# Performance work log

Hardware: AMD Instinct MI355X
Metric: run time of the kernel (lower is better)

The kernel has to match this reference:

```python
import jax, jax.numpy as jnp
import numpy as np

N, E, F, H, O, R = 50000, 600000, 128, 128, 64, 8


def setup_inputs() -> dict:
    key = jax.random.key(0)
    ks = jax.random.split(key, 10)
    x = jax.random.normal(ks[0], (N, F), dtype=jnp.float32)
    edge_index = jax.random.randint(ks[1], (2, E), 0, N, dtype=jnp.int64)
    edge_weight = jax.random.uniform(ks[2], (E,), dtype=jnp.float32)
    edge_type = jax.random.randint(ks[3], (E,), 0, R, dtype=jnp.int64)
    s = 1.0 / np.sqrt(F)
    W1 = jax.random.uniform(ks[4], (R, F, H), jnp.float32, -s, s)
    root1 = jax.random.uniform(ks[5], (F, H), jnp.float32, -s, s)
    bias1 = jnp.zeros((H,), jnp.float32)
    sh = 1.0 / np.sqrt(H)
    W2 = jax.random.uniform(ks[6], (R, H, O), jnp.float32, -sh, sh)
    root2 = jax.random.uniform(ks[7], (H, O), jnp.float32, -sh, sh)
    bias2 = jnp.zeros((O,), jnp.float32)
    return {"x": x, "edge_index": edge_index, "edge_weight": edge_weight,
            "edge_type": edge_type, "W1": W1, "root1": root1, "bias1": bias1,
            "W2": W2, "root2": root2, "bias2": bias2}


def _rgcn_conv(x, src, dst, et, ew, W, root, bias, num_nodes):
    # project every node by every relation: [N, R, out] (cheaper than per-edge
    # materialization of weight[edge_type] which is E x in x out)
    proj = jnp.einsum('nd,rdo->nro', x, W)
    # per-edge message = x_j @ W[edge_type] * edge_weight  -> [E, out]
    msg = proj[src, et] * ew[:, None]
    # weighted scatter-mean over destination nodes
    agg = jax.ops.segment_sum(msg, dst, num_segments=num_nodes)
    cnt = jax.ops.segment_sum(jnp.ones_like(ew), dst, num_segments=num_nodes)
    agg = agg / jnp.maximum(cnt, 1.0)[:, None]
    # root (self) transform + bias
    return agg + x @ root + bias


def reference(x, edge_index, edge_weight, edge_type, W1, root1, bias1, W2, root2, bias2):
    src, dst = edge_index[0], edge_index[1]
    et = edge_type.astype(jnp.int32)
    # min-max normalize edge weights as in RGCN.forward
    ew = (edge_weight - edge_weight.min()) / (edge_weight.max() - edge_weight.min() + 1e-8)
    n = x.shape[0]
    h = jax.nn.relu(_rgcn_conv(x, src, dst, et, ew, W1, root1, bias1, n))
    return _rgcn_conv(h, src, dst, et, ew, W2, root2, bias2, n)
```

## Files before the change

kernel.cpp:

```cpp
#include <hip/hip_runtime.h>
#include <hip/hip_bf16.h>

#define F_DIM 128
#define H_DIM 128
#define O_DIM 64
#define R_NUM 8

typedef __attribute__((ext_vector_type(8))) short bf16x8;
typedef __attribute__((ext_vector_type(4))) float f32x4;
typedef __attribute__((ext_vector_type(8))) unsigned short u16x8;

union V8 { bf16x8 v; short4 h[2]; };

__device__ __forceinline__ unsigned short f2b(float f) {
    unsigned u = __float_as_uint(f);
    u += 0x7FFFu + ((u >> 16) & 1u);
    return (unsigned short)(u >> 16);
}
__device__ __forceinline__ unsigned f2b2(float lo, float hi) {
    union { __hip_bfloat162 h; unsigned u; } p;
    p.h = __float22bfloat162_rn(make_float2(lo, hi));
    return p.u;
}
__device__ __forceinline__ unsigned short f2b1(float f) {
    union { __hip_bfloat16 h; unsigned short u; } p;
    p.h = __float2bfloat16(f);
    return p.u;
}
__device__ __forceinline__ float b2f(unsigned short b) {
    return __uint_as_float(((unsigned)b) << 16);
}

__global__ __launch_bounds__(256) void setupA(
    const float* __restrict__ ew, const int* __restrict__ dst,
    const int* __restrict__ et, int E, int* __restrict__ deg2,
    float* __restrict__ bmn, float* __restrict__ bmx,
    const float* __restrict__ x, unsigned short* __restrict__ xb, long x4,
    const float* __restrict__ W1, const float* __restrict__ root1,
    const float* __restrict__ W2, const float* __restrict__ root2,
    unsigned short* __restrict__ wt1, unsigned short* __restrict__ wt2) {
    __shared__ float smn[256], smx[256];
    const int tid = threadIdx.x;
    const int gstride = gridDim.x * blockDim.x;
    int g0 = blockIdx.x * blockDim.x + tid;

    float mn = 1e30f, mx = -1e30f;
    for (int i = g0; i < E; i += gstride) {
        atomicAdd(&deg2[dst[i] * R_NUM + et[i]], 1);
        float v = ew[i];
        mn = fminf(mn, v);
        mx = fmaxf(mx, v);
    }
    smn[tid] = mn; smx[tid] = mx;
    __syncthreads();
    for (int s = 128; s > 0; s >>= 1) {
        if (tid < s) {
            smn[tid] = fminf(smn[tid], smn[tid + s]);
            smx[tid] = fmaxf(smx[tid], smx[tid + s]);
        }
        __syncthreads();
    }
    if (tid == 0) { bmn[blockIdx.x] = smn[0]; bmx[blockIdx.x] = smx[0]; }

    for (long i = g0; i < x4; i += gstride) {
        float4 v = ((const float4*)x)[i];
        uint2 o = make_uint2(f2b2(v.x, v.y), f2b2(v.z, v.w));
        ((uint2*)xb)[i] = o;
    }

    const int n1 = 9 * 128 * 128, n2 = 9 * 64 * 128;
    for (int idx = g0; idx < n1 + n2; idx += gstride) {
        if (idx < n1) {
            int r = idx / (128 * 128), rem = idx % (128 * 128);
            int n = rem / 128, k = rem % 128;
            float v = (r < 8) ? W1[((size_t)r * 128 + k) * 128 + n]
                              : root1[(size_t)k * 128 + n];
            wt1[idx] = f2b1(v);
        } else {
            int j = idx - n1;
            int r = j / (64 * 128), rem = j % (64 * 128);
            int n = rem / 128, k = rem % 128;
            float v = (r < 8) ? W2[((size_t)r * 128 + k) * 64 + n]
                              : root2[(size_t)k * 64 + n];
            wt2[j] = f2b1(v);
        }
    }
}

__global__ void scan1_kernel(const int* __restrict__ deg, int* __restrict__ rp,
                             int* __restrict__ bsum, float* __restrict__ invc,
                             int M, int N) {
    __shared__ int s[256];
    int base = blockIdx.x * 2048;
    int t = threadIdx.x;
    int v[8]; int loc = 0;
#pragma unroll
    for (int i = 0; i < 8; ++i) {
        int idx = base + t * 8 + i;
        v[i] = (idx < M) ? deg[idx] : 0;
        loc += v[i];
    }
    int node = blockIdx.x * 256 + t;
    if (node < N) invc[node] = 1.0f / (float)max(loc, 1);
    s[t] = loc;
    __syncthreads();
    for (int off = 1; off < 256; off <<= 1) {
        int x = (t >= off) ? s[t - off] : 0;
        __syncthreads();
        s[t] += x;
        __syncthreads();
    }
    int run = s[t] - loc;
#pragma unroll
    for (int i = 0; i < 8; ++i) {
        int idx = base + t * 8 + i;
        if (idx < M) rp[idx] = run;
        run += v[i];
    }
    if (t == 255) bsum[blockIdx.x] = s[255];
}

__global__ void scan2_mm(int* bsum, int nb, const float* __restrict__ bmn,
                         const float* __restrict__ bmx, float* mm) {
    __shared__ int s[256];
    __shared__ float smn[256], smx[256];
    int t = threadIdx.x;
    int v = (t < nb) ? bsum[t] : 0;
    s[t] = v;
    smn[t] = fminf(bmn[t], bmn[t + 256]);
    smx[t] = fmaxf(bmx[t], bmx[t + 256]);
    __syncthreads();
    for (int off = 1; off < 256; off <<= 1) {
        int x = (t >= off) ? s[t - off] : 0;
        __syncthreads();
        s[t] += x;
        __syncthreads();
    }
    if (t < nb) bsum[t] = s[t] - v;
    for (int r = 128; r > 0; r >>= 1) {
        if (t < r) {
            smn[t] = fminf(smn[t], smn[t + r]);
            smx[t] = fmaxf(smx[t], smx[t + r]);
        }
        __syncthreads();
    }
    if (t == 0) { mm[0] = smn[0]; mm[1] = smx[0]; }
}

__global__ void fill2_kernel(const int* __restrict__ src, const int* __restrict__ dst,
                             const int* __restrict__ et, const float* __restrict__ ew,
                             const float* __restrict__ mm, const float* __restrict__ invc,
                             int* __restrict__ rp2, const int* __restrict__ bsum,
                             unsigned* __restrict__ erec, int E) {
    int e = blockIdx.x * blockDim.x + threadIdx.x;
    if (e >= E) return;
    int d = dst[e];
    int i = d * R_NUM + et[e];
    int pos = atomicAdd(&rp2[i], 1) + bsum[i >> 11];
    float mn = mm[0], mx = mm[1];
    unsigned wq = f2b((ew[e] - mn) / (mx - mn + 1e-8f) * invc[d]);
    erec[pos] = (wq << 17) | (unsigned)src[e];
}

__global__ __launch_bounds__(256) void gather_y(
    const int* __restrict__ rp2, const int* __restrict__ bsum,
    const unsigned* __restrict__ erec,
    const unsigned short* __restrict__ inp,
    unsigned short* __restrict__ y, int N) {
    int gid = blockIdx.x * 256 + threadIdx.x;
    int seg = gid >> 4;
    int n = seg >> 3;
    if (n >= N) return;
    int j = (gid & 15) * 8;
    int beg = (seg == 0) ? 0 : rp2[seg - 1] + bsum[(seg - 1) >> 11];
    int end = rp2[seg] + bsum[seg >> 11];
    float acc[8] = {0.f, 0.f, 0.f, 0.f, 0.f, 0.f, 0.f, 0.f};
    int k = beg;
    for (; k + 2 <= end; k += 2) {
        unsigned r0 = erec[k], r1 = erec[k + 1];
        float w0 = __uint_as_float((r0 >> 1) & 0x7FFF8000u);
        float w1 = __uint_as_float((r1 >> 1) & 0x7FFF8000u);
        u16x8 v0 = *(const u16x8*)(inp + (size_t)(r0 & 0x1FFFFu) * 128 + j);
        u16x8 v1 = *(const u16x8*)(inp + (size_t)(r1 & 0x1FFFFu) * 128 + j);
#pragma unroll
        for (int c = 0; c < 8; ++c) acc[c] += w0 * b2f(v0[c]);
#pragma unroll
        for (int c = 0; c < 8; ++c) acc[c] += w1 * b2f(v1[c]);
    }
    if (k < end) {
        unsigned r0 = erec[k];
        float w0 = __uint_as_float((r0 >> 1) & 0x7FFF8000u);
        u16x8 v0 = *(const u16x8*)(inp + (size_t)(r0 & 0x1FFFFu) * 128 + j);
#pragma unroll
        for (int c = 0; c < 8; ++c) acc[c] += w0 * b2f(v0[c]);
    }
    uint4 ov = make_uint4(f2b2(acc[0], acc[1]), f2b2(acc[2], acc[3]),
                          f2b2(acc[4], acc[5]), f2b2(acc[6], acc[7]));
    *(uint4*)(y + ((size_t)(seg & 7) * N + (size_t)n) * 128 + j) = ov;
}

__global__ __launch_bounds__(512, 4) void gemm_y2(
    const unsigned short* __restrict__ y,
    const unsigned short* __restrict__ inp,
    const unsigned short* __restrict__ Wt,
    const float* __restrict__ bias,
    unsigned short* __restrict__ outb, int N)
{
    __shared__ unsigned short smem[2 * 128 * 132];

    const int tid = threadIdx.x;
    const int w = tid >> 6, lane = tid & 63;
    const int quad = lane >> 4, l15 = lane & 15;
    const int n0 = blockIdx.x * 128;

    V8 st[4];
    int srow[4], sseg[4];
#pragma unroll
    for (int it = 0; it < 4; ++it) {
        int u = tid + it * 512;
        srow[it] = u >> 4;
        sseg[it] = u & 15;
    }

    auto issue = [&](int r) {
#pragma unroll
        for (int it = 0; it < 4; ++it) {
            int node = n0 + srow[it];
            if (node >= N) node = N - 1;
            const unsigned short* src = (r < 8)
                ? y + ((size_t)r * N + (size_t)node) * 128 + sseg[it] * 8
                : inp + (size_t)node * 128 + sseg[it] * 8;
            st[it].v = *(const bf16x8*)src;
        }
    };

    f32x4 acc[8];
#pragma unroll
    for (int g = 0; g < 8; ++g) acc[g] = (f32x4){0.f, 0.f, 0.f, 0.f};

    issue(0);

    for (int r = 0; r < 9; ++r) {
        unsigned short* ysb = smem + (r & 1) * (128 * 132);
#pragma unroll
        for (int it = 0; it < 4; ++it) {
            *(short4*)&ysb[srow[it] * 132 + sseg[it] * 8]     = st[it].h[0];
            *(short4*)&ysb[srow[it] * 132 + sseg[it] * 8 + 4] = st[it].h[1];
        }
        if (r < 8) issue(r + 1);
        const unsigned short* wbase = Wt + (size_t)r * 128 * 128;
        bf16x8 afr[4];
#pragma unroll
        for (int k2 = 0; k2 < 4; ++k2) {
            afr[k2] = *(const bf16x8*)(wbase
                + (size_t)(w * 16 + l15) * 128 + k2 * 32 + quad * 8);
        }
        asm volatile("s_waitcnt lgkmcnt(0)" ::: "memory");
        __builtin_amdgcn_s_barrier();

#pragma unroll
        for (int k2 = 0; k2 < 4; ++k2) {
#pragma unroll
            for (int g = 0; g < 8; ++g) {
                const unsigned short* yr = ysb + (size_t)(g * 16 + l15) * 132
                                           + k2 * 32 + quad * 8;
                V8 b;
                b.h[0] = *(const short4*)yr;
                b.h[1] = *(const short4*)(yr + 4);
                acc[g] = __builtin_amdgcn_mfma_f32_16x16x32_bf16(afr[k2], b.v, acc[g], 0, 0, 0);
            }
        }
    }

    __syncthreads();
    unsigned short* stg = smem;
    {
        const int c0 = w * 16 + quad * 4;
        float4 bs = *(const float4*)(bias + c0);
#pragma unroll
        for (int g = 0; g < 8; ++g) {
            float v0 = acc[g][0] + bs.x, v1 = acc[g][1] + bs.y;
            float v2 = acc[g][2] + bs.z, v3 = acc[g][3] + bs.w;
            v0 = fmaxf(v0, 0.f); v1 = fmaxf(v1, 0.f);
            v2 = fmaxf(v2, 0.f); v3 = fmaxf(v3, 0.f);
            uint2 o = make_uint2(f2b2(v0, v1), f2b2(v2, v3));
            *(uint2*)&stg[(g * 16 + l15) * 136 + c0] = o;
        }
    }
    __syncthreads();
    const int gn = tid >> 2, gq = tid & 3;
    const int gnode = n0 + gn;
    if (gnode < N) {
        const unsigned short* srw = stg + gn * 136 + gq * 32;
        unsigned short* drow = outb + (size_t)gnode * 128 + gq * 32;
#pragma unroll
        for (int c = 0; c < 4; ++c)
            *(bf16x8*)(drow + c * 8) = *(const bf16x8*)(srw + c * 8);
    }
}

__global__ __launch_bounds__(256) void gemm_proj2(
    const unsigned short* __restrict__ h,
    const unsigned short* __restrict__ Wt,
    unsigned short* __restrict__ proj2,
    int N)
{
    __shared__ unsigned short hs[64 * 132];
    __shared__ unsigned short wsd[64 * 132];
    __shared__ unsigned short ts[64 * 68];

    const int tid = threadIdx.x;
    const int w = tid >> 6, lane = tid & 63;
    const int quad = lane >> 4, l15 = lane & 15;
    const int n0 = blockIdx.x * 64;

#pragma unroll
    for (int it = 0; it < 4; ++it) {
        int u = tid + it * 256;
        int row = u >> 4, seg = u & 15;
        int node = n0 + row;
        if (node >= N) node = N - 1;
        V8 v; v.v = *(const bf16x8*)(h + (size_t)node * 128 + seg * 8);
        *(short4*)&hs[row * 132 + seg * 8]     = v.h[0];
        *(short4*)&hs[row * 132 + seg * 8 + 4] = v.h[1];
    }

    for (int r = 0; r < 9; ++r) {
#pragma unroll
        for (int it = 0; it < 4; ++it) {
            int u = tid + it * 256;
            int row = u >> 4, seg = u & 15;
            V8 v;
            v.v = *(const bf16x8*)(Wt + ((size_t)r * 64 + row) * 128 + seg * 8);
            *(short4*)&wsd[row * 132 + seg * 8]     = v.h[0];
            *(short4*)&wsd[row * 132 + seg * 8 + 4] = v.h[1];
        }
        __syncthreads();
        f32x4 acc[4];
#pragma unroll
        for (int nt = 0; nt < 4; ++nt) acc[nt] = (f32x4){0.f, 0.f, 0.f, 0.f};
        const unsigned short* yrow = hs + (size_t)(w * 16 + l15) * 132 + quad * 8;
#pragma unroll
        for (int k2 = 0; k2 < 4; ++k2) {
            V8 b;
            b.h[0] = *(const short4*)(yrow + k2 * 32);
            b.h[1] = *(const short4*)(yrow + k2 * 32 + 4);
#pragma unroll
            for (int nt = 0; nt < 4; ++nt) {
                const unsigned short* ar = wsd + (size_t)(nt * 16 + l15) * 132
                                           + k2 * 32 + quad * 8;
                V8 av;
                av.h[0] = *(const short4*)ar;
                av.h[1] = *(const short4*)(ar + 4);
                acc[nt] = __builtin_amdgcn_mfma_f32_16x16x32_bf16(av.v, b.v, acc[nt], 0, 0, 0);
            }
        }
        unsigned short* tw = ts + w * 16 * 68;
#pragma unroll
        for (int nt = 0; nt < 4; ++nt) {
            int c0 = nt * 16 + quad * 4;
            uint2 o = make_uint2(f2b2(acc[nt][0], acc[nt][1]),
                                 f2b2(acc[nt][2], acc[nt][3]));
            *(uint2*)&tw[l15 * 68 + c0] = o;
        }
#pragma unroll
        for (int jj = 0; jj < 2; ++jj) {
            int rl = (lane >> 3) + 8 * jj;
            int off = (lane & 7) * 8;
            int g = n0 + w * 16 + rl;
            V8 v;
            v.h[0] = *(const short4*)&tw[rl * 68 + off];
            v.h[1] = *(const short4*)&tw[rl * 68 + off + 4];
            if (g < N)
                *(bf16x8*)(proj2 + ((size_t)r * N + g) * 64 + off) = v.v;
        }
        __syncthreads();
    }
}

__global__ __launch_bounds__(256) void gather_out2(
    const int* __restrict__ rp2, const int* __restrict__ bsum,
    const unsigned* __restrict__ erec,
    const unsigned short* __restrict__ proj2,
    const float* __restrict__ bias,
    float* __restrict__ out, int N)
{
    int gid = blockIdx.x * 256 + threadIdx.x;
    int n = gid >> 3;
    if (n >= N) return;
    int j = (gid & 7) * 8;

    int base = n * R_NUM;
    int bs_n = bsum[base >> 11];
    int4 ea = *(const int4*)(rp2 + base);
    int4 eb = *(const int4*)(rp2 + base + 4);
    int ends[8] = {ea.x + bs_n, ea.y + bs_n, ea.z + bs_n, ea.w + bs_n,
                   eb.x + bs_n, eb.y + bs_n, eb.z + bs_n, eb.w + bs_n};
    int k = (n == 0) ? 0 : rp2[base - 1] + bsum[(base - 1) >> 11];

    float acc[8] = {0.f, 0.f, 0.f, 0.f, 0.f, 0.f, 0.f, 0.f};
#pragma unroll
    for (int r = 0; r < 8; ++r) {
        int end = ends[r];
        for (; k < end; ++k) {
            unsigned rec = erec[k];
            float wgt = __uint_as_float((rec >> 1) & 0x7FFF8000u);
            u16x8 v = *(const u16x8*)(proj2 + ((size_t)r * N + (rec & 0x1FFFFu)) * 64 + j);
#pragma unroll
            for (int c = 0; c < 8; ++c) acc[c] += wgt * b2f(v[c]);
        }
    }
    u16x8 sv = *(const u16x8*)(proj2 + ((size_t)8 * N + n) * 64 + j);
    float4 b0 = *(const float4*)(bias + j);
    float4 b1 = *(const float4*)(bias + j + 4);
    float* o = out + (size_t)n * 64 + j;
    o[0] = acc[0] + b2f(sv[0]) + b0.x;
    o[1] = acc[1] + b2f(sv[1]) + b0.y;
    o[2] = acc[2] + b2f(sv[2]) + b0.z;
    o[3] = acc[3] + b2f(sv[3]) + b0.w;
    o[4] = acc[4] + b2f(sv[4]) + b1.x;
    o[5] = acc[5] + b2f(sv[5]) + b1.y;
    o[6] = acc[6] + b2f(sv[6]) + b1.z;
    o[7] = acc[7] + b2f(sv[7]) + b1.w;
}

extern "C" void kernel_launch(void* const* d_in, const int* in_sizes, int n_in,
                              void* d_out, int out_size, void* d_ws, size_t ws_size,
                              hipStream_t stream) {
    const float* x     = (const float*)d_in[0];
    const int*   ei    = (const int*)d_in[1];
    const float* ew    = (const float*)d_in[2];
    const int*   et    = (const int*)d_in[3];
    const float* W1    = (const float*)d_in[4];
    const float* root1 = (const float*)d_in[5];
    const float* bias1 = (const float*)d_in[6];
    const float* W2    = (const float*)d_in[7];
    const float* root2 = (const float*)d_in[8];
    const float* bias2 = (const float*)d_in[9];

    const int N = in_sizes[0] / F_DIM;
    const int E = in_sizes[2];
    const int M2 = N * R_NUM;
    const int* srcp = ei;
    const int* dstp = ei + E;

    int* base = (int*)d_ws;
    float* mm    = (float*)base;
    float* invc  = (float*)(base + 16);
    int*   deg2  = base + 16 + N;
    int*   rp2   = deg2 + M2;
    int*   bsum  = rp2 + M2;
    float* bmn   = (float*)(bsum + 256);
    float* bmx   = bmn + 512;
    unsigned* erec = (unsigned*)(bmx + 512);
    unsigned short* xb  = (unsigned short*)(erec + E);
    unsigned short* hb  = xb + (size_t)N * 128;
    unsigned short* wt1 = hb + (size_t)N * 128;
    unsigned short* wt2 = wt1 + 9 * 128 * 128;
    unsigned short* y   = wt2 + 9 * 64 * 128;
    unsigned short* proj2 = y;

    const int TB = 256;
    int blocksE = (E + TB - 1) / TB;
    int nb = (M2 + 2047) / 2048;
    long x4 = (long)N * 128 / 4;

    (void)hipMemsetAsync(deg2, 0, (size_t)M2 * sizeof(int), stream);
    setupA<<<512, TB, 0, stream>>>(ew, dstp, et, E, deg2, bmn, bmx,
                                   x, xb, x4, W1, root1, W2, root2, wt1, wt2);
    scan1_kernel<<<nb, TB, 0, stream>>>(deg2, rp2, bsum, invc, M2, N);
    scan2_mm<<<1, TB, 0, stream>>>(bsum, nb, bmn, bmx, mm);
    fill2_kernel<<<blocksE, TB, 0, stream>>>(srcp, dstp, et, ew, mm, invc,
                                             rp2, bsum, erec, E);

    int gatB = (int)(((long)M2 * 16 + TB - 1) / TB);
    int gB = (N + 63) / 64;
    int gB1 = (N + 127) / 128;

    gather_y<<<gatB, TB, 0, stream>>>(rp2, bsum, erec, xb, y, N);
    gemm_y2<<<gB1, 512, 0, stream>>>(y, xb, wt1, bias1, hb, N);

    gemm_proj2<<<gB, TB, 0, stream>>>(hb, wt2, proj2, N);
    int g2B = (int)(((long)N * 8 + TB - 1) / TB);
    gather_out2<<<g2B, TB, 0, stream>>>(rp2, bsum, erec, proj2, bias2,
                                        (float*)d_out, N);
}
```

Measured before the change: 286.5 us.

## Project before gathering in layer one, fusing root, bias and ReLU into gather

Layer one now projects each node's features by all relation weights and the root weight first (gemm_proj1), writing the root result back in place into xb. A new gather_h kernel then sums the pre-projected rows per node and adds root, bias and ReLU. This replaces the earlier gather-then-GEMM order and removes the 9-way K-accumulating GEMM over the y buffer. In exchange the per-relation projection output must be written and then gathered, which costs the same bandwidth as y, and each gather thread now walks all 8 relation segments serially.

```diff
diff --git a/kernel.cpp b/kernel.cpp
--- a/kernel.cpp
+++ b/kernel.cpp
@@ -162,92 +162,35 @@
     erec[pos] = (wq << 17) | (unsigned)src[e];
 }
 
-__global__ __launch_bounds__(256) void gather_y(
-    const int* __restrict__ rp2, const int* __restrict__ bsum,
-    const unsigned* __restrict__ erec,
-    const unsigned short* __restrict__ inp,
-    unsigned short* __restrict__ y, int N) {
-    int gid = blockIdx.x * 256 + threadIdx.x;
-    int seg = gid >> 4;
-    int n = seg >> 3;
-    if (n >= N) return;
-    int j = (gid & 15) * 8;
-    int beg = (seg == 0) ? 0 : rp2[seg - 1] + bsum[(seg - 1) >> 11];
-    int end = rp2[seg] + bsum[seg >> 11];
-    float acc[8] = {0.f, 0.f, 0.f, 0.f, 0.f, 0.f, 0.f, 0.f};
-    int k = beg;
-    for (; k + 2 <= end; k += 2) {
-        unsigned r0 = erec[k], r1 = erec[k + 1];
-        float w0 = __uint_as_float((r0 >> 1) & 0x7FFF8000u);
-        float w1 = __uint_as_float((r1 >> 1) & 0x7FFF8000u);
-        u16x8 v0 = *(const u16x8*)(inp + (size_t)(r0 & 0x1FFFFu) * 128 + j);
-        u16x8 v1 = *(const u16x8*)(inp + (size_t)(r1 & 0x1FFFFu) * 128 + j);
-#pragma unroll
-        for (int c = 0; c < 8; ++c) acc[c] += w0 * b2f(v0[c]);
-#pragma unroll
-        for (int c = 0; c < 8; ++c) acc[c] += w1 * b2f(v1[c]);
-    }
-    if (k < end) {
-        unsigned r0 = erec[k];
-        float w0 = __uint_as_float((r0 >> 1) & 0x7FFF8000u);
-        u16x8 v0 = *(const u16x8*)(inp + (size_t)(r0 & 0x1FFFFu) * 128 + j);
-#pragma unroll
-        for (int c = 0; c < 8; ++c) acc[c] += w0 * b2f(v0[c]);
-    }
-    uint4 ov = make_uint4(f2b2(acc[0], acc[1]), f2b2(acc[2], acc[3]),
-                          f2b2(acc[4], acc[5]), f2b2(acc[6], acc[7]));
-    *(uint4*)(y + ((size_t)(seg & 7) * N + (size_t)n) * 128 + j) = ov;
-}
-
-__global__ __launch_bounds__(512, 4) void gemm_y2(
-    const unsigned short* __restrict__ y,
-    const unsigned short* __restrict__ inp,
+__global__ __launch_bounds__(512, 4) void gemm_proj1(
+    unsigned short* __restrict__ xb,
     const unsigned short* __restrict__ Wt,
-    const float* __restrict__ bias,
-    unsigned short* __restrict__ outb, int N)
+    unsigned short* __restrict__ proj1,
+    int N)
 {
-    __shared__ unsigned short smem[2 * 128 * 132];
+    __shared__ unsigned short xs[128 * 132];
+    __shared__ unsigned short ts[8 * 128 * 18];
 
     const int tid = threadIdx.x;
     const int w = tid >> 6, lane = tid & 63;
     const int quad = lane >> 4, l15 = lane & 15;
     const int n0 = blockIdx.x * 128;
 
-    V8 st[4];
-    int srow[4], sseg[4];
 #pragma unroll
     for (int it = 0; it < 4; ++it) {
         int u = tid + it * 512;
-        srow[it] = u >> 4;
-        sseg[it] = u & 15;
-    }
-
-    auto issue = [&](int r) {
-#pragma unroll
-        for (int it = 0; it < 4; ++it) {
-            int node = n0 + srow[it];
-            if (node >= N) node = N - 1;
-            const unsigned short* src = (r < 8)
-                ? y + ((size_t)r * N + (size_t)node) * 128 + sseg[it] * 8
-                : inp + (size_t)node * 128 + sseg[it] * 8;
-            st[it].v = *(const bf16x8*)src;
-        }
-    };
-
-    f32x4 acc[8];
-#pragma unroll
-    for (int g = 0; g < 8; ++g) acc[g] = (f32x4){0.f, 0.f, 0.f, 0.f};
-
-    issue(0);
+        int row = u >> 4, seg = u & 15;
+        int node = n0 + row;
+        if (node >= N) node = N - 1;
+        V8 v; v.v = *(const bf16x8*)(xb + (size_t)node * 128 + seg * 8);
+        *(short4*)&xs[row * 132 + seg * 8]     = v.h[0];
+        *(short4*)&xs[row * 132 + seg * 8 + 4] = v.h[1];
+    }
+    __syncthreads();
+
+    unsigned short* tw = ts + (size_t)w * 128 * 18;
 
     for (int r = 0; r < 9; ++r) {
-        unsigned short* ysb = smem + (r & 1) * (128 * 132);
-#pragma unroll
-        for (int it = 0; it < 4; ++it) {
-            *(short4*)&ysb[srow[it] * 132 + sseg[it] * 8]     = st[it].h[0];
-            *(short4*)&ysb[srow[it] * 132 + sseg[it] * 8 + 4] = st[it].h[1];
-        }
-        if (r < 8) issue(r + 1);
         const unsigned short* wbase = Wt + (size_t)r * 128 * 128;
         bf16x8 afr[4];
 #pragma unroll
@@ -255,14 +198,14 @@
             afr[k2] = *(const bf16x8*)(wbase
                 + (size_t)(w * 16 + l15) * 128 + k2 * 32 + quad * 8);
         }
-        asm volatile("s_waitcnt lgkmcnt(0)" ::: "memory");
-        __builtin_amdgcn_s_barrier();
-
+        f32x4 acc[8];
+#pragma unroll
+        for (int g = 0; g < 8; ++g) acc[g] = (f32x4){0.f, 0.f, 0.f, 0.f};
 #pragma unroll
         for (int k2 = 0; k2 < 4; ++k2) {
 #pragma unroll
             for (int g = 0; g < 8; ++g) {
-                const unsigned short* yr = ysb + (size_t)(g * 16 + l15) * 132
+                const unsigned short* yr = xs + (size_t)(g * 16 + l15) * 132
                                            + k2 * 32 + quad * 8;
                 V8 b;
                 b.h[0] = *(const short4*)yr;
@@ -270,33 +213,78 @@
                 acc[g] = __builtin_amdgcn_mfma_f32_16x16x32_bf16(afr[k2], b.v, acc[g], 0, 0, 0);
             }
         }
-    }
-
-    __syncthreads();
-    unsigned short* stg = smem;
-    {
-        const int c0 = w * 16 + quad * 4;
-        float4 bs = *(const float4*)(bias + c0);
 #pragma unroll
         for (int g = 0; g < 8; ++g) {
-            float v0 = acc[g][0] + bs.x, v1 = acc[g][1] + bs.y;
-            float v2 = acc[g][2] + bs.z, v3 = acc[g][3] + bs.w;
-            v0 = fmaxf(v0, 0.f); v1 = fmaxf(v1, 0.f);
-            v2 = fmaxf(v2, 0.f); v3 = fmaxf(v3, 0.f);
-            uint2 o = make_uint2(f2b2(v0, v1), f2b2(v2, v3));
-            *(uint2*)&stg[(g * 16 + l15) * 136 + c0] = o;
-        }
-    }
-    __syncthreads();
-    const int gn = tid >> 2, gq = tid & 3;
-    const int gnode = n0 + gn;
-    if (gnode < N) {
-        const unsigned short* srw = stg + gn * 136 + gq * 32;
-        unsigned short* drow = outb + (size_t)gnode * 128 + gq * 32;
-#pragma unroll
-        for (int c = 0; c < 4; ++c)
-            *(bf16x8*)(drow + c * 8) = *(const bf16x8*)(srw + c * 8);
-    }
+            uint2 o = make_uint2(f2b2(acc[g][0], acc[g][1]),
+                                 f2b2(acc[g][2], acc[g][3]));
+            *(uint2*)&tw[(g * 16 + l15) * 18 + quad * 4] = o;
+        }
+#pragma unroll
+        for (int jj = 0; jj < 4; ++jj) {
+            int nd = (lane >> 1) + 32 * jj;
+            int off = (lane & 1) * 8;
+            int g = n0 + nd;
+            V8 v;
+            v.h[0] = *(const short4*)&tw[nd * 18 + off];
+            v.h[1] = *(const short4*)&tw[nd * 18 + off + 4];
+            if (g < N) {
+                unsigned short* dst = (r < 8)
+                    ? proj1 + ((size_t)r * N + g) * 128 + w * 16 + off
+                    : xb + (size_t)g * 128 + w * 16 + off;
+                *(bf16x8*)dst = v.v;
+            }
+        }
+        __syncthreads();
+    }
+}
+
+__global__ __launch_bounds__(256) void gather_h(
+    const int* __restrict__ rp2, const int* __restrict__ bsum,
+    const unsigned* __restrict__ erec,
+    const unsigned short* __restrict__ proj1,
+    const unsigned short* __restrict__ xroot,
+    const float* __restrict__ bias,
+    unsigned short* __restrict__ hb, int N)
+{
+    int gid = blockIdx.x * 256 + threadIdx.x;
+    int n = gid >> 4;
+    if (n >= N) return;
+    int j = (gid & 15) * 8;
+
+    int base = n * R_NUM;
+    int bs_n = bsum[base >> 11];
+    int4 ea = *(const int4*)(rp2 + base);
+    int4 eb = *(const int4*)(rp2 + base + 4);
+    int ends[8] = {ea.x + bs_n, ea.y + bs_n, ea.z + bs_n, ea.w + bs_n,
+                   eb.x + bs_n, eb.y + bs_n, eb.z + bs_n, eb.w + bs_n};
+    int k = (n == 0) ? 0 : rp2[base - 1] + bsum[(base - 1) >> 11];
+
+    float acc[8] = {0.f, 0.f, 0.f, 0.f, 0.f, 0.f, 0.f, 0.f};
+#pragma unroll
+    for (int r = 0; r < 8; ++r) {
+        int end = ends[r];
+        for (; k < end; ++k) {
+            unsigned rec = erec[k];
+            float wgt = __uint_as_float((rec >> 1) & 0x7FFF8000u);
+            u16x8 v = *(const u16x8*)(proj1 + ((size_t)r * N + (rec & 0x1FFFFu)) * 128 + j);
+#pragma unroll
+            for (int c = 0; c < 8; ++c) acc[c] += wgt * b2f(v[c]);
+        }
+    }
+    u16x8 sv = *(const u16x8*)(xroot + (size_t)n * 128 + j);
+    float4 b0 = *(const float4*)(bias + j);
+    float4 b1 = *(const float4*)(bias + j + 4);
+    float o0 = fmaxf(acc[0] + b2f(sv[0]) + b0.x, 0.f);
+    float o1 = fmaxf(acc[1] + b2f(sv[1]) + b0.y, 0.f);
+    float o2 = fmaxf(acc[2] + b2f(sv[2]) + b0.z, 0.f);
+    float o3 = fmaxf(acc[3] + b2f(sv[3]) + b0.w, 0.f);
+    float o4 = fmaxf(acc[4] + b2f(sv[4]) + b1.x, 0.f);
+    float o5 = fmaxf(acc[5] + b2f(sv[5]) + b1.y, 0.f);
+    float o6 = fmaxf(acc[6] + b2f(sv[6]) + b1.z, 0.f);
+    float o7 = fmaxf(acc[7] + b2f(sv[7]) + b1.w, 0.f);
+    uint4 ov = make_uint4(f2b2(o0, o1), f2b2(o2, o3),
+                          f2b2(o4, o5), f2b2(o6, o7));
+    *(uint4*)(hb + (size_t)n * 128 + j) = ov;
 }
 
 __global__ __launch_bounds__(256) void gemm_proj2(
@@ -457,8 +445,8 @@
     unsigned short* hb  = xb + (size_t)N * 128;
     unsigned short* wt1 = hb + (size_t)N * 128;
     unsigned short* wt2 = wt1 + 9 * 128 * 128;
-    unsigned short* y   = wt2 + 9 * 64 * 128;
-    unsigned short* proj2 = y;
+    unsigned short* proj1 = wt2 + 9 * 64 * 128;
+    unsigned short* proj2 = proj1;
 
     const int TB = 256;
     int blocksE = (E + TB - 1) / TB;
@@ -473,12 +461,12 @@
     fill2_kernel<<<blocksE, TB, 0, stream>>>(srcp, dstp, et, ew, mm, invc,
                                              rp2, bsum, erec, E);
 
-    int gatB = (int)(((long)M2 * 16 + TB - 1) / TB);
     int gB = (N + 63) / 64;
     int gB1 = (N + 127) / 128;
 
-    gather_y<<<gatB, TB, 0, stream>>>(rp2, bsum, erec, xb, y, N);
-    gemm_y2<<<gB1, 512, 0, stream>>>(y, xb, wt1, bias1, hb, N);
+    gemm_proj1<<<gB1, 512, 0, stream>>>(xb, wt1, proj1, N);
+    int gHB = (int)(((long)N * 16 + TB - 1) / TB);
+    gather_h<<<gHB, TB, 0, stream>>>(rp2, bsum, erec, proj1, xb, bias1, hb, N);
 
     gemm_proj2<<<gB, TB, 0, stream>>>(hb, wt2, proj2, N);
     int g2B = (int)(((long)N * 8 + TB - 1) / TB);
```

After: 339.0 us. 1.18x slower.
